# Kernel optimization log

Hardware: AMD Instinct MI355X
Metric: run time of the kernel (lower is better)

## Reference

```python
import jax, jax.numpy as jnp
import numpy as np

# dims: L blocks, S cur_seq, M memory_len, B batch, D embed, H heads, IN input_dim
L, S, M, B, D, H, IN = 4, 512, 512, 8, 1024, 16, 128
HD = D // H
GRU_BIAS = 2.0  # config['gru_bias']


def _ln(x, s, b, eps=1e-5):
    mu = x.mean(-1, keepdims=True)
    var = ((x - mu) ** 2).mean(-1, keepdims=True)
    return (x - mu) * jax.lax.rsqrt(var + eps) * s + b


def _pos_emb(full_seq, dim):
    # SinusoidalPE: freqs = arange(0, dim, 2.0); inv = 10000**(-freqs/dim); seq descending
    freqs = jnp.arange(0, dim, 2.0)
    inv = 10000.0 ** (-freqs / dim)
    seq = jnp.arange(full_seq - 1, -1, -1.0)
    ang = seq[:, None] * inv[None, :]
    return jnp.concatenate([jnp.sin(ang), jnp.cos(ang)], axis=-1)  # (F, dim)


def _rel_shift(x):
    # x: (q, k, b, h) -> Transformer-XL relative shift
    q, k, b, h = x.shape
    xp = jnp.pad(x, ((0, 0), (1, 0), (0, 0), (0, 0)))
    return xp.reshape(k + 1, q, b, h)[1:].reshape(q, k, b, h)


def _gru(x, y, Wr, Ur, Wz, Uz, Wg, Ug):
    r = jax.nn.sigmoid(y @ Wr + x @ Ur)
    z = jax.nn.sigmoid(y @ Wz + x @ Uz - GRU_BIAS)
    hcand = jnp.tanh(y @ Wg + (r * x) @ Ug)
    return (1.0 - z) * x + z * hcand


def setup_inputs() -> dict:
    key = jax.random.key(0)
    ks = iter(jax.random.split(key, 64))

    def mat(*shape):
        return jax.random.normal(next(ks), shape, jnp.float32) * (shape[-2] ** -0.5)

    return dict(
        h=jax.random.normal(next(ks), (B, S, IN), jnp.float32),
        memory=jnp.zeros((L, M, B, D), jnp.float32),
        We=mat(IN, D), be=jnp.zeros((D,), jnp.float32),
        ln1_s=jnp.ones((L, D), jnp.float32), ln1_b=jnp.zeros((L, D), jnp.float32),
        ln2_s=jnp.ones((L, D), jnp.float32), ln2_b=jnp.zeros((L, D), jnp.float32),
        Wq=mat(L, D, D), bq=jnp.zeros((L, D), jnp.float32),
        Wk=mat(L, D, D), bk=jnp.zeros((L, D), jnp.float32),
        Wv=mat(L, D, D), bv=jnp.zeros((L, D), jnp.float32),
        Wr=mat(L, D, D), br=jnp.zeros((L, D), jnp.float32),
        Wo=mat(L, D, D), bo=jnp.zeros((L, D), jnp.float32),
        u=jax.random.normal(next(ks), (L, H, HD), jnp.float32) * 0.02,
        vb=jax.random.normal(next(ks), (L, H, HD), jnp.float32) * 0.02,
        gWr=mat(L, 2, D, D), gUr=mat(L, 2, D, D),
        gWz=mat(L, 2, D, D), gUz=mat(L, 2, D, D),
        gWg=mat(L, 2, D, D), gUg=mat(L, 2, D, D),
        fW1=mat(L, D, 4 * D), fb1=jnp.zeros((L, 4 * D), jnp.float32),
        fW2=mat(L, 4 * D, D), fb2=jnp.zeros((L, D), jnp.float32),
    )


def reference(h, memory, We, be, ln1_s, ln1_b, ln2_s, ln2_b,
              Wq, bq, Wk, bk, Wv, bv, Wr, br, Wo, bo, u, vb,
              gWr, gUr, gWz, gUz, gWg, gUg, fW1, fb1, fW2, fb2):
    x = jnp.transpose(h, (1, 0, 2))                      # (S, B, IN)
    x = jax.nn.gelu(x @ We + be, approximate=False)      # (S, B, D)
    F = S + M
    pos = _pos_emb(F, D)                                 # (F, D)
    mask = jnp.triu(jnp.ones((S, F), bool), k=1 + M)     # (S, F)
    scale = HD ** -0.5
    out = x
    for i in range(L):
        full = jnp.concatenate([memory[i], out], axis=0)  # (F, B, D)
        qn = _ln(out, ln1_s[i], ln1_b[i])
        kn = _ln(full, ln1_s[i], ln1_b[i])
        q = (qn @ Wq[i] + bq[i]).reshape(S, B, H, HD)
        k = (kn @ Wk[i] + bk[i]).reshape(F, B, H, HD)
        v = (kn @ Wv[i] + bv[i]).reshape(F, B, H, HD)
        r = (pos @ Wr[i] + br[i]).reshape(F, H, HD)
        content = jnp.einsum('ibhd,jbhd->ijbh', q + u[i], k)
        position = _rel_shift(jnp.einsum('ibhd,jhd->ijbh', q + vb[i], r))
        attn = (content + position) * scale               # (S, F, B, H)
        attn = jnp.where(mask[:, :, None, None], -1e30, attn)
        a = jax.nn.softmax(attn, axis=1)
        y = jnp.einsum('ijbh,jbhd->ibhd', a, v).reshape(S, B, D) @ Wo[i] + bo[i]
        y = jax.nn.gelu(y, approximate=False)
        out1 = _gru(out, y, gWr[i, 0], gUr[i, 0], gWz[i, 0], gUz[i, 0], gWg[i, 0], gUg[i, 0])
        e = _ln(out1, ln2_s[i], ln2_b[i])
        e = jax.nn.gelu(e @ fW1[i] + fb1[i], approximate=False)
        e = jax.nn.gelu(e @ fW2[i] + fb2[i], approximate=False)
        out = _gru(out1, e, gWr[i, 1], gUr[i, 1], gWz[i, 1], gUz[i, 1], gWg[i, 1], gUg[i, 1])
    return jnp.transpose(out, (1, 0, 2))                  # (B, S, D)
```

## Files before the change

kernel.cpp:

```cpp
#include <hip/hip_runtime.h>

typedef unsigned short u16;
typedef unsigned long long u64;
typedef __attribute__((ext_vector_type(8))) short bf16x8;
typedef __attribute__((ext_vector_type(4))) float f32x4;

#define DEVI __device__ __forceinline__

#define KSC 0.1803368801111244f

DEVI u16 f2b(float f) {
  unsigned u = __float_as_uint(f);
  u += 0x7fffu + ((u >> 16) & 1u);
  return (u16)(u >> 16);
}
DEVI float b2f(u16 v) { return __uint_as_float((unsigned)v << 16); }
DEVI unsigned cvtpk(float lo, float hi) {
  unsigned r;
  asm("v_cvt_pk_bf16_f32 %0, %1, %2" : "=v"(r) : "v"(lo), "v"(hi));
  return r;
}
DEVI float tanh_f(float x) {
  float xc = fminf(fmaxf(x, -15.f), 15.f);
  float e = __expf(2.f * xc);
  return (e - 1.f) / (e + 1.f);
}
DEVI float gelu_f(float x) {
  float u = 0.7978845608028654f * x * (1.f + 0.044715f * x * x);
  return 0.5f * x * (1.f + tanh_f(u));
}
DEVI float sigm_f(float x) { return 1.f / (1.f + __expf(-x)); }

DEVI void gload16(const void* g, void* l) {
  __builtin_amdgcn_global_load_lds((__attribute__((address_space(1))) void*)g,
                                   (__attribute__((address_space(3))) void*)l, 16, 0, 0);
}

template <int NT, int BN>
__global__ __launch_bounds__(NT) void gemm_bt(
    const u16* __restrict__ A, const u16* __restrict__ Bt,
    const float* __restrict__ bias, const float* __restrict__ bias2,
    float* __restrict__ C32, u16* __restrict__ C16, u16* __restrict__ C16b,
    int M, int N, int K, int ldA, int ldB, int ldC,
    long long sA, long long sBb, long long sBh, long long sC, int nH, int flags)
{
  constexpr int WN = BN / 32;
  constexpr int RA = (128 * 8) / NT;
  constexpr int RB = (BN * 8) / NT;
  __shared__ __align__(16) u16 Sm[2][(128 + BN) * 64];
  const int z = blockIdx.z;
  const int zb = z / nH, zh = z - zb * nH;
  A  += (long long)z * sA;
  Bt += (long long)zb * sBb + (long long)zh * sBh;
  const long long cOff = (long long)z * sC;
  const int m0 = blockIdx.x * 128, n0 = blockIdx.y * BN;
  const int t = threadIdx.x, lane = t & 63;
  const int w = t >> 6;
  const int wm = (w / WN) * 64, wn = (w % WN) * 32;

  f32x4 acc[4][2];
#pragma unroll
  for (int i = 0; i < 4; ++i)
#pragma unroll
    for (int j = 0; j < 2; ++j) { f32x4 zz = {0.f, 0.f, 0.f, 0.f}; acc[i][j] = zz; }

  auto stage = [&](int buf, int k0) {
#pragma unroll
    for (int r = 0; r < RA; ++r) {
      const int c = r * NT + t;
      const int row = c >> 3;
      const int col = (c & 7) << 3;
      int ga = m0 + row; if (ga >= M) ga = M - 1;
      gload16(A + (long long)ga * ldA + (k0 + col),
              &Sm[buf][(size_t)(r * NT + (t & (NT - 64))) * 8]);
    }
#pragma unroll
    for (int r = 0; r < RB; ++r) {
      const int c = r * NT + t;
      const int row = c >> 3;
      const int col = (c & 7) << 3;
      int gb = n0 + row; if (gb >= N) gb = N - 1;
      gload16(Bt + (long long)gb * ldB + (k0 + col),
              &Sm[buf][(size_t)(1024 + r * NT + (t & (NT - 64))) * 8]);
    }
  };

  auto compute = [&](int buf) {
    const u16* As = &Sm[buf][0];
    const u16* Bs = &Sm[buf][128 * 64];
#pragma unroll
    for (int ks = 0; ks < 2; ++ks) {
      const int ko = ks * 32 + ((lane >> 4) << 3);
      bf16x8 af[4], bfv[2];
#pragma unroll
      for (int i = 0; i < 4; ++i)
        af[i] = *(const bf16x8*)&As[(wm + i * 16 + (lane & 15)) * 64 + ko];
#pragma unroll
      for (int i = 0; i < 2; ++i)
        bfv[i] = *(const bf16x8*)&Bs[(wn + i * 16 + (lane & 15)) * 64 + ko];
#pragma unroll
      for (int mi = 0; mi < 4; ++mi)
#pragma unroll
        for (int ni = 0; ni < 2; ++ni)
          acc[mi][ni] = __builtin_amdgcn_mfma_f32_16x16x32_bf16(af[mi], bfv[ni], acc[mi][ni], 0, 0, 0);
    }
  };

  stage(0, 0);
  __syncthreads();
  int cur = 0;
  for (int k0 = 64; k0 < K; k0 += 64) {
    stage(cur ^ 1, k0);
    compute(cur);
    __syncthreads();
    cur ^= 1;
  }
  compute(cur);

  const int cb = n0 + wn + (lane & 15);
  const int rb = m0 + wm + ((lane >> 4) << 2);
#pragma unroll
  for (int ni = 0; ni < 2; ++ni) {
    const int col = cb + ni * 16;
    if (col >= N) continue;
    float bv = 0.f;
    if (flags & 2) bv = ((flags & 128) && zh) ? bias2[col] : bias[col];
#pragma unroll
    for (int mi = 0; mi < 4; ++mi) {
#pragma unroll
      for (int q = 0; q < 4; ++q) {
        const int row = rb + mi * 16 + q;
        if (row >= M) continue;
        float x = acc[mi][ni][q] + bv;
        if (flags & 1) x = gelu_f(x);
        if (flags & 64) {
          const long long o = ((long long)((row & 7) * 16 + (col >> 6)) * ldC + (row >> 3)) * 64 + (col & 63);
          C16[o] = f2b(x * KSC);
          C16b[o] = f2b((x + bias2[col]) * KSC);
        } else if (flags & 128) {
          if (zh == 0) {
            const long long o = ((long long)((row & 7) * 16 + (col >> 6)) * ldC + (row >> 3)) * 64 + (col & 63);
            C16[o] = f2b(x);
          } else {
            C16b[(long long)row * 1024 + col] = f2b(x);
          }
        } else {
          long long o;
          if (flags & 16)
            o = ((long long)((row & 7) * 16 + (col >> 6)) * ldC + (row >> 3)) * 64 + (col & 63);
          else if (flags & 32)
            o = ((long long)(col >> 6) * 1024 + row) * 64 + (col & 63);
          else
            o = cOff + (long long)row * ldC + col;
          if (flags & 4) C32[o] = x;
          if (flags & 8) C16[o] = f2b(x);
        }
      }
    }
  }
}

__global__ __launch_bounds__(256) void fused_attn(
    const u16* __restrict__ Qu,
    const u16* __restrict__ Qv,
    const u16* __restrict__ Kb,
    const u16* __restrict__ Vt,
    const u16* __restrict__ Rh,
    u16* __restrict__ Y)
{
  constexpr int F = 1024;
  const int bid = blockIdx.x;
  const int wk = (bid & 7) * 128 + (bid >> 3);
  const int i0 = (wk & 7) * 64;
  const int bh = wk >> 3;
  const int h = bh & 15;

  __shared__ __align__(16) u16 Ks[2][64 * 64];
  __shared__ __align__(16) u16 Vs[2][64 * 64];
  __shared__ __align__(16) u16 Rs[2][64 * 64];
  __shared__ __align__(8) u16 PBT[2][64 * 68];
  __shared__ __align__(16) u16 Ps[4][16][72];

  const int t = threadIdx.x;
  const int lane = t & 63;
  const int wq = t >> 6;
  const int l15 = lane & 15, lhi = lane >> 4;

  const u16* QUg = Qu + ((size_t)bh * 512 + i0) * 64;
  const u16* QVg = Qv + ((size_t)bh * 512 + i0) * 64;
  const u16* Kg = Kb + (size_t)bh * F * 64;
  const u16* Vg = Vt + (size_t)bh * 64 * F;
  const u16* Rg = Rh + (size_t)h * F * 64;

  bf16x8 au[2], av[2];
#pragma unroll
  for (int ks = 0; ks < 2; ++ks) {
    const int arow = wq * 16 + l15;
    au[ks] = *(const bf16x8*)(QUg + arow * 64 + ks * 32 + lhi * 8);
    av[ks] = *(const bf16x8*)(QVg + arow * 64 + ks * 32 + lhi * 8);
  }

  auto stageT = [&](const u16* g, u16* dst) {
#pragma unroll
    for (int rnd = 0; rnd < 2; ++rnd) {
      const int idx = rnd * 256 + t;
      const int row = idx >> 3;
      const int gs = (idx & 7) ^ (row & 7);
      gload16(g + row * 64 + gs * 8, dst + (size_t)(rnd * 256 + (t & 192)) * 8);
    }
  };
  auto stageVf = [&](int j0, u16* dst) {
#pragma unroll
    for (int rnd = 0; rnd < 2; ++rnd) {
      const int idx = rnd * 256 + t;
      const int row = idx >> 3;
      const int gs = (idx & 7) ^ (row & 7);
      gload16(Vg + (size_t)row * F + j0 + gs * 8, dst + (size_t)(rnd * 256 + (t & 192)) * 8);
    }
  };

  const int nT = i0 / 64 + 9;

  stageT(Kg, Ks[0]);
  stageVf(0, Vs[0]);
  stageT(Rg + (size_t)(512 - i0) * 64, Rs[0]);
  stageT(Rg + (size_t)(448 - i0) * 64, Rs[1]);
  __syncthreads();
  {
    f32x4 pb0[4];
#pragma unroll
    for (int i = 0; i < 4; ++i) { f32x4 zz = {0.f, 0.f, 0.f, 0.f}; pb0[i] = zz; }
    __builtin_amdgcn_s_setprio(1);
#pragma unroll
    for (int ks = 0; ks < 2; ++ks)
#pragma unroll
      for (int ni = 0; ni < 4; ++ni) {
        const int brow = ni * 16 + l15;
        const bf16x8 br_ = *(const bf16x8*)&Rs[1][brow * 64 + (((ks * 4 + lhi) ^ (brow & 7)) << 3)];
        pb0[ni] = __builtin_amdgcn_mfma_f32_16x16x32_bf16(av[ks], br_, pb0[ni], 0, 0, 0);
      }
    __builtin_amdgcn_s_setprio(0);
#pragma unroll
    for (int ni = 0; ni < 4; ++ni) {
      u64 w = (u64)cvtpk(pb0[ni][0], pb0[ni][1]) | ((u64)cvtpk(pb0[ni][2], pb0[ni][3]) << 32);
      *(u64*)&PBT[0][(size_t)(ni * 16 + l15) * 68 + wq * 16 + lhi * 4] = w;
    }
  }
  __syncthreads();

  f32x4 Oacc[4];
#pragma unroll
  for (int i = 0; i < 4; ++i) { f32x4 zz = {0.f, 0.f, 0.f, 0.f}; Oacc[i] = zz; }
  float mrow[4] = {-3.0e38f, -3.0e38f, -3.0e38f, -3.0e38f};
  float lrow[4] = {0.f, 0.f, 0.f, 0.f};

  for (int st = 0; st < nT; ++st) {
    const int b = st & 1;
    const bool lastT = (st == nT - 1);

    if (!lastT) {
      const int j1 = (st + 1) * 64;
      stageT(Kg + (size_t)j1 * 64, Ks[b ^ 1]);
      stageVf(j1, Vs[b ^ 1]);
      if (st + 1 < nT - 1)
        stageT(Rg + (size_t)(j1 - i0 + 512) * 64, Rs[b ^ 1]);
    }

    f32x4 cacc[4], pbh[4];
#pragma unroll
    for (int i = 0; i < 4; ++i) {
      f32x4 zz = {0.f, 0.f, 0.f, 0.f};
      cacc[i] = zz; pbh[i] = zz;
    }
    __builtin_amdgcn_s_setprio(1);
#pragma unroll
    for (int ks = 0; ks < 2; ++ks) {
#pragma unroll
      for (int ni = 0; ni < 4; ++ni) {
        const int brow = ni * 16 + l15;
        const bf16x8 bk_ = *(const bf16x8*)&Ks[b][brow * 64 + (((ks * 4 + lhi) ^ (brow & 7)) << 3)];
        cacc[ni] = __builtin_amdgcn_mfma_f32_16x16x32_bf16(au[ks], bk_, cacc[ni], 0, 0, 0);
      }
      if (!lastT) {
#pragma unroll
        for (int ni = 0; ni < 4; ++ni) {
          const int brow = ni * 16 + l15;
          const bf16x8 br_ = *(const bf16x8*)&Rs[b][brow * 64 + (((ks * 4 + lhi) ^ (brow & 7)) << 3)];
          pbh[ni] = __builtin_amdgcn_mfma_f32_16x16x32_bf16(av[ks], br_, pbh[ni], 0, 0, 0);
        }
      }
    }
    __builtin_amdgcn_s_setprio(0);

    if (!lastT) {
#pragma unroll
      for (int ni = 0; ni < 4; ++ni) {
        u64 w = (u64)cvtpk(pbh[ni][0], pbh[ni][1]) | ((u64)cvtpk(pbh[ni][2], pbh[ni][3]) << 32);
        *(u64*)&PBT[(st + 1) & 1][(size_t)(ni * 16 + l15) * 68 + wq * 16 + lhi * 4] = w;
      }
    }

    const u16* pbLo = &PBT[st & 1][0];
    const u16* pbHi = &PBT[(st + 1) & 1][0];
    float sc[4][4];
#pragma unroll
    for (int ni = 0; ni < 4; ++ni) {
      const int dj = ni * 16 + l15;
#pragma unroll
      for (int qq = 0; qq < 4; ++qq) {
        const int di = wq * 16 + lhi * 4 + qq;
        const int cc = dj - di + 63;
        const float pb = b2f((cc < 64) ? pbLo[(size_t)cc * 68 + di]
                                       : pbHi[(size_t)(cc - 64) * 68 + di]);
        float s = cacc[ni][qq] + pb;
        if (lastT && dj > di) s = -1e30f;
        sc[ni][qq] = s;
      }
    }

    float nm[4], esc[4];
#pragma unroll
    for (int qq = 0; qq < 4; ++qq) {
      float r = fmaxf(fmaxf(sc[0][qq], sc[1][qq]), fmaxf(sc[2][qq], sc[3][qq]));
      r = fmaxf(r, __shfl_xor(r, 1));
      r = fmaxf(r, __shfl_xor(r, 2));
      r = fmaxf(r, __shfl_xor(r, 4));
      r = fmaxf(r, __shfl_xor(r, 8));
      nm[qq] = fmaxf(mrow[qq], r);
      esc[qq] = exp2f(mrow[qq] - nm[qq]);
      mrow[qq] = nm[qq];
    }
    float ps[4][4];
    float rsum[4] = {0.f, 0.f, 0.f, 0.f};
#pragma unroll
    for (int ni = 0; ni < 4; ++ni)
#pragma unroll
      for (int qq = 0; qq < 4; ++qq) {
        float p = exp2f(sc[ni][qq] - nm[qq]);
        ps[ni][qq] = p;
        rsum[qq] += p;
      }
#pragma unroll
    for (int qq = 0; qq < 4; ++qq) {
      float r = rsum[qq];
      r += __shfl_xor(r, 1);
      r += __shfl_xor(r, 2);
      r += __shfl_xor(r, 4);
      r += __shfl_xor(r, 8);
      lrow[qq] = lrow[qq] * esc[qq] + r;
    }
#pragma unroll
    for (int nd = 0; nd < 4; ++nd)
#pragma unroll
      for (int qq = 0; qq < 4; ++qq) Oacc[nd][qq] *= esc[qq];

#pragma unroll
    for (int ni = 0; ni < 4; ++ni) {
      unsigned p01 = cvtpk(ps[ni][0], ps[ni][1]);
      unsigned p23 = cvtpk(ps[ni][2], ps[ni][3]);
      Ps[wq][lhi * 4 + 0][ni * 16 + l15] = (u16)p01;
      Ps[wq][lhi * 4 + 1][ni * 16 + l15] = (u16)(p01 >> 16);
      Ps[wq][lhi * 4 + 2][ni * 16 + l15] = (u16)p23;
      Ps[wq][lhi * 4 + 3][ni * 16 + l15] = (u16)(p23 >> 16);
    }
    __builtin_amdgcn_s_setprio(1);
#pragma unroll
    for (int ks = 0; ks < 2; ++ks) {
      const bf16x8 pa = *(const bf16x8*)&Ps[wq][l15][ks * 32 + lhi * 8];
#pragma unroll
      for (int nd = 0; nd < 4; ++nd) {
        const int vrow = nd * 16 + l15;
        const bf16x8 vb_ = *(const bf16x8*)&Vs[b][vrow * 64 + (((ks * 4 + lhi) ^ (vrow & 7)) << 3)];
        Oacc[nd] = __builtin_amdgcn_mfma_f32_16x16x32_bf16(pa, vb_, Oacc[nd], 0, 0, 0);
      }
    }
    __builtin_amdgcn_s_setprio(0);

    __syncthreads();
  }

  float inv[4];
#pragma unroll
  for (int qq = 0; qq < 4; ++qq) inv[qq] = 1.f / lrow[qq];
  const int b = bh >> 4;
  const int rbase = i0 + wq * 16 + lhi * 4;
#pragma unroll
  for (int nd = 0; nd < 4; ++nd) {
    const int d = nd * 16 + l15;
    unsigned w01 = cvtpk(Oacc[nd][0] * inv[0], Oacc[nd][1] * inv[1]);
    unsigned w23 = cvtpk(Oacc[nd][2] * inv[2], Oacc[nd][3] * inv[3]);
    u16* yb = Y + (size_t)rbase * 8192 + b * 1024 + h * 64 + d;
    yb[0] = (u16)w01; yb[8192] = (u16)(w01 >> 16);
    yb[16384] = (u16)w23; yb[24576] = (u16)(w23 >> 16);
  }
}

__global__ __launch_bounds__(256) void biasprep(const float* __restrict__ bq,
                                                const float* __restrict__ u,
                                                const float* __restrict__ vb,
                                                float* __restrict__ bqu,
                                                float* __restrict__ dvb)
{
  const int i = blockIdx.x * 256 + threadIdx.x;
  bqu[i] = bq[i] + u[i];
  dvb[i] = vb[i] - u[i];
}

#define MAXW 20
struct WPack {
  const float* src[MAXW];
  u16* dst[MAXW];
  int K[MAXW], N[MAXW];
  int tilePrefix[MAXW + 1];
  int nm;
};

__global__ __launch_bounds__(256) void wtrans_kernel(WPack p) {
  int bid = blockIdx.x;
  int m = 0;
  while (m < p.nm && bid >= p.tilePrefix[m + 1]) ++m;
  if (m >= p.nm) return;
  const int lt = bid - p.tilePrefix[m];
  const int K = p.K[m], N = p.N[m];
  const int tN = N >> 5;
  const int kt = lt / tN, nt = lt - kt * tN;
  const int k0 = kt << 5, n0 = nt << 5;
  const float* src = p.src[m];
  u16* dst = p.dst[m];
  __shared__ float tile[32][33];
  const int t = threadIdx.x;
  const int r = t >> 3, c4 = (t & 7) << 2;
  float4 v = *(const float4*)&src[(size_t)(k0 + r) * N + n0 + c4];
  tile[r][c4 + 0] = v.x; tile[r][c4 + 1] = v.y; tile[r][c4 + 2] = v.z; tile[r][c4 + 3] = v.w;
  __syncthreads();
  u16 o0 = f2b(tile[c4 + 0][r]);
  u16 o1 = f2b(tile[c4 + 1][r]);
  u16 o2 = f2b(tile[c4 + 2][r]);
  u16 o3 = f2b(tile[c4 + 3][r]);
  u64 w = (u64)o0 | ((u64)o1 << 16) | ((u64)o2 << 32) | ((u64)o3 << 48);
  *(u64*)&dst[(size_t)(n0 + r) * K + k0 + c4] = w;
}

__global__ __launch_bounds__(256) void ln_kernel(
    const float* __restrict__ Xmem, const float* __restrict__ Xout, int rowsMem,
    const float* __restrict__ sc, const float* __restrict__ bi, u16* __restrict__ dst)
{
  const int row = blockIdx.x;
  const float* src = (row < rowsMem) ? (Xmem + (long long)row * 1024)
                                     : (Xout + (long long)(row - rowsMem) * 1024);
  const int t = threadIdx.x;
  float4 v = *(const float4*)&src[t * 4];
  float s1 = v.x + v.y + v.z + v.w;
  float s2 = v.x * v.x + v.y * v.y + v.z * v.z + v.w * v.w;
#pragma unroll
  for (int o = 32; o > 0; o >>= 1) { s1 += __shfl_down(s1, o); s2 += __shfl_down(s2, o); }
  __shared__ float red[8];
  const int wv = t >> 6;
  if ((t & 63) == 0) { red[wv * 2] = s1; red[wv * 2 + 1] = s2; }
  __syncthreads();
  s1 = red[0] + red[2] + red[4] + red[6];
  s2 = red[1] + red[3] + red[5] + red[7];
  const float mu = s1 * (1.f / 1024.f);
  const float var = s2 * (1.f / 1024.f) - mu * mu;
  const float rs = rsqrtf(var + 1e-5f);
  float vals[4] = {v.x, v.y, v.z, v.w};
  u16 o4[4];
#pragma unroll
  for (int j = 0; j < 4; ++j) {
    const int c = t * 4 + j;
    o4[j] = f2b((vals[j] - mu) * rs * sc[c] + bi[c]);
  }
  *(u64*)&dst[(long long)row * 1024 + t * 4] =
      (u64)o4[0] | ((u64)o4[1] << 16) | ((u64)o4[2] << 32) | ((u64)o4[3] << 48);
}

__global__ __launch_bounds__(256) void prep_vt16(const u16* __restrict__ Vf, u16* __restrict__ VT)
{
  const int f0 = blockIdx.x * 64;
  const int bh = blockIdx.y;
  const int b = bh >> 4, h = bh & 15;
  __shared__ u16 tl[64 * 64];
  const int t = threadIdx.x;
  {
    const int fr = t >> 2, c0 = (t & 3) * 16;
    const u16* src = Vf + ((size_t)(f0 + fr) * 8 + b) * 1024 + h * 64 + c0;
    *(bf16x8*)&tl[fr * 64 + c0] = *(const bf16x8*)src;
    *(bf16x8*)&tl[fr * 64 + c0 + 8] = *(const bf16x8*)(src + 8);
  }
  __syncthreads();
  {
    const int dr = t >> 2, c0 = (t & 3) * 16;
    u16* dst = VT + ((long long)bh * 64 + dr) * 1024 + f0 + c0;
#pragma unroll
    for (int j = 0; j < 16; ++j) dst[j] = tl[(c0 + j) * 64 + dr];
  }
}

__global__ __launch_bounds__(256) void pe_kernel(u16* __restrict__ PEB)
{
  const long long idx = (long long)blockIdx.x * 256 + threadIdx.x;
  const int p = (int)(idx >> 10);
  const int d = idx & 1023;
  const int q = d & 511;
  const float inv = powf(10000.f, -(float)(2 * q) * (1.f / 1024.f));
  const float ang = (float)(1023 - p) * inv;
  PEB[idx] = f2b((d < 512) ? sinf(ang) : cosf(ang));
}

__global__ __launch_bounds__(256) void embed_conv(const float* __restrict__ h, u16* __restrict__ A)
{
  const long long idx = (long long)blockIdx.x * 256 + threadIdx.x;
  const int c = idx & 127;
  const int r = (int)(idx >> 7);
  const int s = r >> 3, b = r & 7;
  A[idx] = f2b(h[(((long long)b * 512 + s) << 7) + c]);
}

__global__ __launch_bounds__(256) void gru_elemA(const u16* __restrict__ T1, u16* __restrict__ T2,
                                                 const float* __restrict__ X, u16* __restrict__ RXBF)
{
  const long long i8 = ((long long)blockIdx.x * 256 + threadIdx.x) * 8;
  const int row = (int)(i8 >> 10);
  const int c = i8 & 1023;
  const u16* t1 = T1 + (long long)row * 3072 + c;
  u16* t2 = T2 + (long long)row * 2048 + c;
  bf16x8 ry = *(const bf16x8*)t1;
  bf16x8 zy = *(const bf16x8*)(t1 + 1024);
  bf16x8 rx = *(const bf16x8*)t2;
  bf16x8 zx = *(const bf16x8*)(t2 + 1024);
  float4 x0 = *(const float4*)(X + i8);
  float4 x1 = *(const float4*)(X + i8 + 4);
  float xs[8] = {x0.x, x0.y, x0.z, x0.w, x1.x, x1.y, x1.z, x1.w};
  u16 ro[8], zo[8];
#pragma unroll
  for (int j = 0; j < 8; ++j) {
    float r = sigm_f(b2f((u16)ry[j]) + b2f((u16)rx[j]));
    float z = sigm_f(b2f((u16)zy[j]) + b2f((u16)zx[j]) - 2.f);
    ro[j] = f2b(r * xs[j]);
    zo[j] = f2b(z);
  }
  *(u64*)&RXBF[i8] = (u64)ro[0] | ((u64)ro[1] << 16) | ((u64)ro[2] << 32) | ((u64)ro[3] << 48);
  *(u64*)&RXBF[i8 + 4] = (u64)ro[4] | ((u64)ro[5] << 16) | ((u64)ro[6] << 32) | ((u64)ro[7] << 48);
  *(u64*)&t2[0] = (u64)zo[0] | ((u64)zo[1] << 16) | ((u64)zo[2] << 32) | ((u64)zo[3] << 48);
  *(u64*)&t2[4] = (u64)zo[4] | ((u64)zo[5] << 16) | ((u64)zo[6] << 32) | ((u64)zo[7] << 48);
}

__global__ __launch_bounds__(256) void gru_elemB(const u16* __restrict__ T1, const u16* __restrict__ T2,
                                                 const u16* __restrict__ TG, const float* __restrict__ X,
                                                 float* __restrict__ O, u16* __restrict__ XBF)
{
  const long long i8 = ((long long)blockIdx.x * 256 + threadIdx.x) * 8;
  const int row = (int)(i8 >> 10);
  const int c = i8 & 1023;
  bf16x8 gy = *(const bf16x8*)(T1 + (long long)row * 3072 + 2048 + c);
  bf16x8 tt = *(const bf16x8*)(TG + i8);
  bf16x8 zz = *(const bf16x8*)(T2 + (long long)row * 2048 + c);
  float4 x0 = *(const float4*)(X + i8);
  float4 x1 = *(const float4*)(X + i8 + 4);
  float xs[8] = {x0.x, x0.y, x0.z, x0.w, x1.x, x1.y, x1.z, x1.w};
  float os[8];
  u16 ob[8];
#pragma unroll
  for (int j = 0; j < 8; ++j) {
    float z = b2f((u16)zz[j]);
    float o = (1.f - z) * xs[j] + z * tanh_f(b2f((u16)gy[j]) + b2f((u16)tt[j]));
    os[j] = o;
    ob[j] = f2b(o);
  }
  float4 o0 = {os[0], os[1], os[2], os[3]};
  float4 o1 = {os[4], os[5], os[6], os[7]};
  *(float4*)(O + i8) = o0;
  *(float4*)(O + i8 + 4) = o1;
  *(u64*)&XBF[i8] = (u64)ob[0] | ((u64)ob[1] << 16) | ((u64)ob[2] << 32) | ((u64)ob[3] << 48);
  *(u64*)&XBF[i8 + 4] = (u64)ob[4] | ((u64)ob[5] << 16) | ((u64)ob[6] << 32) | ((u64)ob[7] << 48);
}

__global__ __launch_bounds__(256) void out_transpose(const float* __restrict__ O, float* __restrict__ dst)
{
  const long long i4 = ((long long)blockIdx.x * 256 + threadIdx.x) * 4;
  const int d = i4 & 1023;
  const int r = (int)(i4 >> 10);
  const int s = r >> 3, b = r & 7;
  float4 v = *(const float4*)(O + i4);
  *(float4*)&dst[(((long long)b * 512 + s) << 10) + d] = v;
}

extern "C" void kernel_launch(void* const* d_in, const int* in_sizes, int n_in,
                              void* d_out, int out_size, void* d_ws, size_t ws_size,
                              hipStream_t stream)
{
  (void)in_sizes; (void)n_in; (void)out_size; (void)ws_size;
  const float* h_in   = (const float*)d_in[0];
  const float* memory = (const float*)d_in[1];
  const float* We     = (const float*)d_in[2];
  const float* be     = (const float*)d_in[3];
  const float* ln1s   = (const float*)d_in[4];
  const float* ln1b   = (const float*)d_in[5];
  const float* ln2s   = (const float*)d_in[6];
  const float* ln2b   = (const float*)d_in[7];
  const float* Wq     = (const float*)d_in[8];
  const float* bq     = (const float*)d_in[9];
  const float* Wk     = (const float*)d_in[10];
  const float* bk     = (const float*)d_in[11];
  const float* Wv     = (const float*)d_in[12];
  const float* bv     = (const float*)d_in[13];
  const float* Wr     = (const float*)d_in[14];
  const float* br     = (const float*)d_in[15];
  const float* Wo     = (const float*)d_in[16];
  const float* bo     = (const float*)d_in[17];
  const float* uu     = (const float*)d_in[18];
  const float* vbp    = (const float*)d_in[19];
  const float* gWr    = (const float*)d_in[20];
  const float* gUr    = (const float*)d_in[21];
  const float* gWz    = (const float*)d_in[22];
  const float* gUz    = (const float*)d_in[23];
  const float* gWg    = (const float*)d_in[24];
  const float* gUg    = (const float*)d_in[25];
  const float* fW1    = (const float*)d_in[26];
  const float* fb1    = (const float*)d_in[27];
  const float* fW2    = (const float*)d_in[28];
  const float* fb2    = (const float*)d_in[29];

  constexpr int S = 512, MM = 512, B = 8, D = 1024, H = 16, IN = 128, F = 1024;
  constexpr int SB = 4096, FB = 8192;
  constexpr long long DD = (long long)D * D;

  char* ws = (char*)d_ws;
  size_t off = 0;
  auto alloc = [&](size_t bytes) -> size_t {
    size_t o = off; off = (off + bytes + 255) & ~(size_t)255; return o;
  };
  const size_t oWT   = alloc((size_t)25 * DD * 2);
  const size_t oWET  = alloc((size_t)D * IN * 2);
  const size_t oPEB  = alloc((size_t)F * D * 2);
  const size_t oOUT  = alloc((size_t)SB * D * 4);
  const size_t oOUT1 = alloc((size_t)SB * D * 4);
  const size_t oXBF  = alloc((size_t)SB * D * 2);
  const size_t oYBF  = alloc((size_t)SB * D * 2);
  const size_t oYBFA = alloc((size_t)SB * D * 2);
  const size_t oABUF = alloc((size_t)SB * D * 2);
  const size_t oKN   = alloc((size_t)FB * D * 2);
  const size_t oQU   = alloc((size_t)B * H * S * 64 * 2);
  const size_t oQV   = alloc((size_t)B * H * S * 64 * 2);
  const size_t oKBH  = alloc((size_t)B * H * F * 64 * 2);
  const size_t oVT   = alloc((size_t)B * H * F * 64 * 2);
  const size_t oRH   = alloc((size_t)H * F * 64 * 2);
  const size_t oBQU  = alloc((size_t)D * 4);
  const size_t oDVB  = alloc((size_t)D * 4);
  const size_t oUNI  = off;

  u16* WTp   = (u16*)(ws + oWT);
  u16* WETp  = (u16*)(ws + oWET);
  u16* PEBp  = (u16*)(ws + oPEB);
  float* OUTp  = (float*)(ws + oOUT);
  float* OUT1p = (float*)(ws + oOUT1);
  u16* XBFp  = (u16*)(ws + oXBF);
  u16* YBFp  = (u16*)(ws + oYBF);
  u16* YBFAp = (u16*)(ws + oYBFA);
  u16* ABUFp = (u16*)(ws + oABUF);
  u16* KNp   = (u16*)(ws + oKN);
  u16* QUp   = (u16*)(ws + oQU);
  u16* QVp   = (u16*)(ws + oQV);
  u16* KBHp  = (u16*)(ws + oKBH);
  u16* VTp   = (u16*)(ws + oVT);
  u16* RHp   = (u16*)(ws + oRH);
  float* bquP = (float*)(ws + oBQU);
  float* dvbP = (float*)(ws + oDVB);
  u16* VF16p  = (u16*)(ws + oUNI);
  u16* T1p    = (u16*)(ws + oUNI);
  u16* T2p    = (u16*)(ws + oUNI + (size_t)SB * 3 * D * 2 + 256);
  u16* TGp    = (u16*)(ws + oUNI + (size_t)SB * 5 * D * 2 + 512);
  u16* FFNBp  = (u16*)(ws + oUNI);

  auto gemm = [&](const u16* A, const u16* Bt, const float* bias, const float* bias2,
                  float* C32, u16* C16, u16* C16b,
                  int M, int N, int K, int ldA, int ldB, int ldC,
                  long long sA, long long sBb, long long sBh, long long sC, int nH, int Z,
                  int flags) {
    if (M >= 2048 && N >= 1024 && (N % 128) == 0) {
      dim3 grid((M + 127) / 128, N / 128, Z);
      gemm_bt<512, 128><<<grid, 512, 0, stream>>>(A, Bt, bias, bias2, C32, C16, C16b,
                                                  M, N, K, ldA, ldB, ldC,
                                                  sA, sBb, sBh, sC, nH, flags);
    } else {
      dim3 grid((M + 127) / 128, (N + 63) / 64, Z);
      gemm_bt<256, 64><<<grid, 256, 0, stream>>>(A, Bt, bias, bias2, C32, C16, C16b,
                                                 M, N, K, ldA, ldB, ldC,
                                                 sA, sBb, sBh, sC, nH, flags);
    }
  };

  pe_kernel<<<(F * D) / 256, 256, 0, stream>>>(PEBp);
  {
    WPack p{};
    p.nm = 1; p.src[0] = We; p.dst[0] = WETp; p.K[0] = IN; p.N[0] = D;
    p.tilePrefix[0] = 0; p.tilePrefix[1] = (IN / 32) * (D / 32);
    wtrans_kernel<<<p.tilePrefix[1], 256, 0, stream>>>(p);
  }
  embed_conv<<<(SB * IN) / 256, 256, 0, stream>>>(h_in, ABUFp);
  gemm(ABUFp, WETp, be, nullptr, OUTp, XBFp, nullptr, SB, D, IN, IN, IN, D,
       0, 0, 0, 0, 1, 1, 1 | 2 | 4 | 8);

  for (int li = 0; li < 4; ++li) {
    WPack p{};
    int nt = 0, id = 0;
    auto addw = [&](const float* s, u16* d, int K, int N) {
      p.src[id] = s; p.dst[id] = d; p.K[id] = K; p.N[id] = N;
      p.tilePrefix[id] = nt; nt += (K / 32) * (N / 32); ++id;
    };
    addw(Wq + li * DD, WTp + 0 * DD, D, D);
    addw(Wk + li * DD, WTp + 1 * DD, D, D);
    addw(Wv + li * DD, WTp + 2 * DD, D, D);
    addw(Wr + li * DD, WTp + 3 * DD, D, D);
    addw(Wo + li * DD, WTp + 4 * DD, D, D);
    addw(gWr + (li * 2 + 0) * DD, WTp + 5 * DD, D, D);
    addw(gWz + (li * 2 + 0) * DD, WTp + 6 * DD, D, D);
    addw(gWg + (li * 2 + 0) * DD, WTp + 7 * DD, D, D);
    addw(gUr + (li * 2 + 0) * DD, WTp + 8 * DD, D, D);
    addw(gUz + (li * 2 + 0) * DD, WTp + 9 * DD, D, D);
    addw(gUg + (li * 2 + 0) * DD, WTp + 10 * DD, D, D);
    addw(gWr + (li * 2 + 1) * DD, WTp + 11 * DD, D, D);
    addw(gWz + (li * 2 + 1) * DD, WTp + 12 * DD, D, D);
    addw(gWg + (li * 2 + 1) * DD, WTp + 13 * DD, D, D);
    addw(gUr + (li * 2 + 1) * DD, WTp + 14 * DD, D, D);
    addw(gUz + (li * 2 + 1) * DD, WTp + 15 * DD, D, D);
    addw(gUg + (li * 2 + 1) * DD, WTp + 16 * DD, D, D);
    addw(fW1 + li * (long long)D * 4096, WTp + 17 * DD, D, 4096);
    addw(fW2 + li * (long long)4096 * D, WTp + 21 * DD, 4096, D);
    p.tilePrefix[id] = nt; p.nm = id;
    wtrans_kernel<<<nt, 256, 0, stream>>>(p);

    ln_kernel<<<FB, 256, 0, stream>>>(memory + (long long)li * MM * B * D, OUTp, MM * B,
                                      ln1s + li * D, ln1b + li * D, KNp);
    const u16* QN = KNp + (size_t)MM * B * D;

    biasprep<<<4, 256, 0, stream>>>(bq + li * D, uu + li * D, vbp + li * D, bquP, dvbP);
    gemm(QN, WTp + 0 * DD, bquP, dvbP, nullptr, QUp, QVp, SB, D, D, D, D,  S,
         0, 0, 0, 0, 1, 1, 2 | 64);
    gemm(KNp, WTp + 1 * DD, bk + li * D, bv + li * D, nullptr, KBHp, VF16p,
         FB, D, D, D, D,  F, 0, 0, DD, 0, 2, 2, 2 | 128);
    prep_vt16<<<dim3(F / 64, B * H), 256, 0, stream>>>(VF16p, VTp);
    gemm(PEBp, WTp + 3 * DD, br + li * D, nullptr, nullptr, RHp, nullptr,
         F, D, D, D, D, D, 0, 0, 0, 0, 1, 1, 2 | 8 | 32);

    fused_attn<<<dim3((S / 64) * B * H), 256, 0, stream>>>(QUp, QVp, KBHp, VTp, RHp, YBFAp);

    gemm(YBFAp, WTp + 4 * DD, bo + li * D, nullptr, nullptr, YBFp, nullptr,
         SB, D, D, D, D, D, 0, 0, 0, 0, 1, 1, 1 | 2 | 8);

    gemm(YBFp, WTp + 5 * DD, nullptr, nullptr, nullptr, T1p, nullptr,
         SB, 3 * D, D, D, D, 3 * D, 0, 0, 0, 0, 1, 1, 8);
    gemm(XBFp, WTp + 8 * DD, nullptr, nullptr, nullptr, T2p, nullptr,
         SB, 2 * D, D, D, D, 2 * D, 0, 0, 0, 0, 1, 1, 8);
    gru_elemA<<<(SB * D / 8) / 256, 256, 0, stream>>>(T1p, T2p, OUTp, ABUFp);
    gemm(ABUFp, WTp + 10 * DD, nullptr, nullptr, nullptr, TGp, nullptr,
         SB, D, D, D, D, D, 0, 0, 0, 0, 1, 1, 8);
    gru_elemB<<<(SB * D / 8) / 256, 256, 0, stream>>>(T1p, T2p, TGp, OUTp, OUT1p, XBFp);

    ln_kernel<<<SB, 256, 0, stream>>>(OUT1p, OUT1p, SB, ln2s + li * D, ln2b + li * D, ABUFp);
    gemm(ABUFp, WTp + 17 * DD, fb1 + li * 4096, nullptr, nullptr, FFNBp, nullptr,
         SB, 4096, D, D, D, 4096, 0, 0, 0, 0, 1, 1, 1 | 2 | 8);
    gemm(FFNBp, WTp + 21 * DD, fb2 + li * D, nullptr, nullptr, YBFp, nullptr,
         SB, D, 4096, 4096, 4096, D, 0, 0, 0, 0, 1, 1, 1 | 2 | 8);

    gemm(YBFp, WTp + 11 * DD, nullptr, nullptr, nullptr, T1p, nullptr,
         SB, 3 * D, D, D, D, 3 * D, 0, 0, 0, 0, 1, 1, 8);
    gemm(XBFp, WTp + 14 * DD, nullptr, nullptr, nullptr, T2p, nullptr,
         SB, 2 * D, D, D, D, 2 * D, 0, 0, 0, 0, 1, 1, 8);
    gru_elemA<<<(SB * D / 8) / 256, 256, 0, stream>>>(T1p, T2p, OUT1p, ABUFp);
    gemm(ABUFp, WTp + 16 * DD, nullptr, nullptr, nullptr, TGp, nullptr,
         SB, D, D, D, D, D, 0, 0, 0, 0, 1, 1, 8);
    gru_elemB<<<(SB * D / 8) / 256, 256, 0, stream>>>(T1p, T2p, TGp, OUT1p, OUTp, XBFp);
  }

  out_transpose<<<(SB * D / 4) / 256, 256, 0, stream>>>(OUTp, (float*)d_out);
}
```

Before: 2.887 ms.

## Fuse GRU gate elementwise ops and output transpose into GEMM epilogues

The GRU r/z gate computation moves into the epilogue of the U-projection GEMM, and the candidate/blend step into the epilogue of the Ug GEMM. This removes the gru_elemA/gru_elemB kernels and the intermediate T2/TG buffers. On the last layer the output permutation to (B,S,D) is written directly from the epilogue, so out_transpose is dropped. In exchange, the epilogues now do scalar non-vectorized gathers from E1/EX, which could cost more per element than the vectorized standalone kernels.

Measured after the change: 3.091 ms. 1.07x slower.

```diff
diff --git a/kernel.cpp b/kernel.cpp
--- a/kernel.cpp
+++ b/kernel.cpp
@@ -40,6 +40,8 @@
 __global__ __launch_bounds__(NT) void gemm_bt(
     const u16* __restrict__ A, const u16* __restrict__ Bt,
     const float* __restrict__ bias, const float* __restrict__ bias2,
+    const u16* __restrict__ E1, const u16* __restrict__ E2,
+    const float* __restrict__ EX,
     float* __restrict__ C32, u16* __restrict__ C16, u16* __restrict__ C16b,
     int M, int N, int K, int ldA, int ldB, int ldC,
     long long sA, long long sBb, long long sBh, long long sC, int nH, int flags)
@@ -133,7 +135,28 @@
         if (row >= M) continue;
         float x = acc[mi][ni][q] + bv;
         if (flags & 1) x = gelu_f(x);
-        if (flags & 64) {
+        if (flags & 256) {
+          const float t1v = b2f(E1[(size_t)row * 3072 + col]);
+          if (col < 1024) {
+            const float r = sigm_f(x + t1v);
+            C16[(size_t)row * 1024 + col] = f2b(r * EX[(size_t)row * 1024 + col]);
+          } else {
+            const float zv = sigm_f(x + t1v - 2.f);
+            C16b[(size_t)row * 1024 + col - 1024] = f2b(zv);
+          }
+        } else if (flags & 512) {
+          const float gy = b2f(E1[(size_t)row * 3072 + 2048 + col]);
+          const float zv = b2f(E2[(size_t)row * 1024 + col]);
+          const float xv = EX[(size_t)row * 1024 + col];
+          const float o = (1.f - zv) * xv + zv * tanh_f(x + gy);
+          long long oo;
+          if (flags & 1024)
+            oo = ((((long long)(row & 7) * 512 + (row >> 3))) << 10) + col;
+          else
+            oo = (long long)row * 1024 + col;
+          C32[oo] = o;
+          C16[(size_t)row * 1024 + col] = f2b(o);
+        } else if (flags & 64) {
           const long long o = ((long long)((row & 7) * 16 + (col >> 6)) * ldC + (row >> 3)) * 64 + (col & 63);
           C16[o] = f2b(x * KSC);
           C16b[o] = f2b((x + bias2[col]) * KSC);
@@ -514,75 +537,6 @@
   const int r = (int)(idx >> 7);
   const int s = r >> 3, b = r & 7;
   A[idx] = f2b(h[(((long long)b * 512 + s) << 7) + c]);
-}
-
-__global__ __launch_bounds__(256) void gru_elemA(const u16* __restrict__ T1, u16* __restrict__ T2,
-                                                 const float* __restrict__ X, u16* __restrict__ RXBF)
-{
-  const long long i8 = ((long long)blockIdx.x * 256 + threadIdx.x) * 8;
-  const int row = (int)(i8 >> 10);
-  const int c = i8 & 1023;
-  const u16* t1 = T1 + (long long)row * 3072 + c;
-  u16* t2 = T2 + (long long)row * 2048 + c;
-  bf16x8 ry = *(const bf16x8*)t1;
-  bf16x8 zy = *(const bf16x8*)(t1 + 1024);
-  bf16x8 rx = *(const bf16x8*)t2;
-  bf16x8 zx = *(const bf16x8*)(t2 + 1024);
-  float4 x0 = *(const float4*)(X + i8);
-  float4 x1 = *(const float4*)(X + i8 + 4);
-  float xs[8] = {x0.x, x0.y, x0.z, x0.w, x1.x, x1.y, x1.z, x1.w};
-  u16 ro[8], zo[8];
-#pragma unroll
-  for (int j = 0; j < 8; ++j) {
-    float r = sigm_f(b2f((u16)ry[j]) + b2f((u16)rx[j]));
-    float z = sigm_f(b2f((u16)zy[j]) + b2f((u16)zx[j]) - 2.f);
-    ro[j] = f2b(r * xs[j]);
-    zo[j] = f2b(z);
-  }
-  *(u64*)&RXBF[i8] = (u64)ro[0] | ((u64)ro[1] << 16) | ((u64)ro[2] << 32) | ((u64)ro[3] << 48);
-  *(u64*)&RXBF[i8 + 4] = (u64)ro[4] | ((u64)ro[5] << 16) | ((u64)ro[6] << 32) | ((u64)ro[7] << 48);
-  *(u64*)&t2[0] = (u64)zo[0] | ((u64)zo[1] << 16) | ((u64)zo[2] << 32) | ((u64)zo[3] << 48);
-  *(u64*)&t2[4] = (u64)zo[4] | ((u64)zo[5] << 16) | ((u64)zo[6] << 32) | ((u64)zo[7] << 48);
-}
-
-__global__ __launch_bounds__(256) void gru_elemB(const u16* __restrict__ T1, const u16* __restrict__ T2,
-                                                 const u16* __restrict__ TG, const float* __restrict__ X,
-                                                 float* __restrict__ O, u16* __restrict__ XBF)
-{
-  const long long i8 = ((long long)blockIdx.x * 256 + threadIdx.x) * 8;
-  const int row = (int)(i8 >> 10);
-  const int c = i8 & 1023;
-  bf16x8 gy = *(const bf16x8*)(T1 + (long long)row * 3072 + 2048 + c);
-  bf16x8 tt = *(const bf16x8*)(TG + i8);
-  bf16x8 zz = *(const bf16x8*)(T2 + (long long)row * 2048 + c);
-  float4 x0 = *(const float4*)(X + i8);
-  float4 x1 = *(const float4*)(X + i8 + 4);
-  float xs[8] = {x0.x, x0.y, x0.z, x0.w, x1.x, x1.y, x1.z, x1.w};
-  float os[8];
-  u16 ob[8];
-#pragma unroll
-  for (int j = 0; j < 8; ++j) {
-    float z = b2f((u16)zz[j]);
-    float o = (1.f - z) * xs[j] + z * tanh_f(b2f((u16)gy[j]) + b2f((u16)tt[j]));
-    os[j] = o;
-    ob[j] = f2b(o);
-  }
-  float4 o0 = {os[0], os[1], os[2], os[3]};
-  float4 o1 = {os[4], os[5], os[6], os[7]};
-  *(float4*)(O + i8) = o0;
-  *(float4*)(O + i8 + 4) = o1;
-  *(u64*)&XBF[i8] = (u64)ob[0] | ((u64)ob[1] << 16) | ((u64)ob[2] << 32) | ((u64)ob[3] << 48);
-  *(u64*)&XBF[i8 + 4] = (u64)ob[4] | ((u64)ob[5] << 16) | ((u64)ob[6] << 32) | ((u64)ob[7] << 48);
-}
-
-__global__ __launch_bounds__(256) void out_transpose(const float* __restrict__ O, float* __restrict__ dst)
-{
-  const long long i4 = ((long long)blockIdx.x * 256 + threadIdx.x) * 4;
-  const int d = i4 & 1023;
-  const int r = (int)(i4 >> 10);
-  const int s = r >> 3, b = r & 7;
-  float4 v = *(const float4*)(O + i4);
-  *(float4*)&dst[(((long long)b * 512 + s) << 10) + d] = v;
 }
 
 extern "C" void kernel_launch(void* const* d_in, const int* in_sizes, int n_in,
@@ -639,6 +593,7 @@
   const size_t oYBF  = alloc((size_t)SB * D * 2);
   const size_t oYBFA = alloc((size_t)SB * D * 2);
   const size_t oABUF = alloc((size_t)SB * D * 2);
+  const size_t oT2Z  = alloc((size_t)SB * D * 2);
   const size_t oKN   = alloc((size_t)FB * D * 2);
   const size_t oQU   = alloc((size_t)B * H * S * 64 * 2);
   const size_t oQV   = alloc((size_t)B * H * S * 64 * 2);
@@ -658,6 +613,7 @@
   u16* YBFp  = (u16*)(ws + oYBF);
   u16* YBFAp = (u16*)(ws + oYBFA);
   u16* ABUFp = (u16*)(ws + oABUF);
+  u16* T2Zp  = (u16*)(ws + oT2Z);
   u16* KNp   = (u16*)(ws + oKN);
   u16* QUp   = (u16*)(ws + oQU);
   u16* QVp   = (u16*)(ws + oQV);
@@ -668,24 +624,23 @@
   float* dvbP = (float*)(ws + oDVB);
   u16* VF16p  = (u16*)(ws + oUNI);
   u16* T1p    = (u16*)(ws + oUNI);
-  u16* T2p    = (u16*)(ws + oUNI + (size_t)SB * 3 * D * 2 + 256);
-  u16* TGp    = (u16*)(ws + oUNI + (size_t)SB * 5 * D * 2 + 512);
-  u16* FFNBp  = (u16*)(ws + oUNI);
+  u16* FFNBp  = (u16*)(ws + oUNI + (size_t)SB * 3 * D * 2 + 256);
 
   auto gemm = [&](const u16* A, const u16* Bt, const float* bias, const float* bias2,
+                  const u16* E1, const u16* E2, const float* EX,
                   float* C32, u16* C16, u16* C16b,
                   int M, int N, int K, int ldA, int ldB, int ldC,
                   long long sA, long long sBb, long long sBh, long long sC, int nH, int Z,
                   int flags) {
     if (M >= 2048 && N >= 1024 && (N % 128) == 0) {
       dim3 grid((M + 127) / 128, N / 128, Z);
-      gemm_bt<512, 128><<<grid, 512, 0, stream>>>(A, Bt, bias, bias2, C32, C16, C16b,
-                                                  M, N, K, ldA, ldB, ldC,
+      gemm_bt<512, 128><<<grid, 512, 0, stream>>>(A, Bt, bias, bias2, E1, E2, EX,
+                                                  C32, C16, C16b, M, N, K, ldA, ldB, ldC,
                                                   sA, sBb, sBh, sC, nH, flags);
     } else {
       dim3 grid((M + 127) / 128, (N + 63) / 64, Z);
-      gemm_bt<256, 64><<<grid, 256, 0, stream>>>(A, Bt, bias, bias2, C32, C16, C16b,
-                                                 M, N, K, ldA, ldB, ldC,
+      gemm_bt<256, 64><<<grid, 256, 0, stream>>>(A, Bt, bias, bias2, E1, E2, EX,
+                                                 C32, C16, C16b, M, N, K, ldA, ldB, ldC,
                                                  sA, sBb, sBh, sC, nH, flags);
     }
   };
@@ -698,8 +653,8 @@
     wtrans_kernel<<<p.tilePrefix[1], 256, 0, stream>>>(p);
   }
   embed_conv<<<(SB * IN) / 256, 256, 0, stream>>>(h_in, ABUFp);
-  gemm(ABUFp, WETp, be, nullptr, OUTp, XBFp, nullptr, SB, D, IN, IN, IN, D,
-       0, 0, 0, 0, 1, 1, 1 | 2 | 4 | 8);
+  gemm(ABUFp, WETp, be, nullptr, nullptr, nullptr, nullptr, OUTp, XBFp, nullptr,
+       SB, D, IN, IN, IN, D, 0, 0, 0, 0, 1, 1, 1 | 2 | 4 | 8);
 
   for (int li = 0; li < 4; ++li) {
     WPack p{};
@@ -735,43 +690,38 @@
     const u16* QN = KNp + (size_t)MM * B * D;
 
     biasprep<<<4, 256, 0, stream>>>(bq + li * D, uu + li * D, vbp + li * D, bquP, dvbP);
-    gemm(QN, WTp + 0 * DD, bquP, dvbP, nullptr, QUp, QVp, SB, D, D, D, D,  S,
-         0, 0, 0, 0, 1, 1, 2 | 64);
-    gemm(KNp, WTp + 1 * DD, bk + li * D, bv + li * D, nullptr, KBHp, VF16p,
-         FB, D, D, D, D,  F, 0, 0, DD, 0, 2, 2, 2 | 128);
+    gemm(QN, WTp + 0 * DD, bquP, dvbP, nullptr, nullptr, nullptr, nullptr, QUp, QVp,
+         SB, D, D, D, D,  S, 0, 0, 0, 0, 1, 1, 2 | 64);
+    gemm(KNp, WTp + 1 * DD, bk + li * D, bv + li * D, nullptr, nullptr, nullptr,
+         nullptr, KBHp, VF16p, FB, D, D, D, D,  F, 0, 0, DD, 0, 2, 2, 2 | 128);
     prep_vt16<<<dim3(F / 64, B * H), 256, 0, stream>>>(VF16p, VTp);
-    gemm(PEBp, WTp + 3 * DD, br + li * D, nullptr, nullptr, RHp, nullptr,
-         F, D, D, D, D, D, 0, 0, 0, 0, 1, 1, 2 | 8 | 32);
+    gemm(PEBp, WTp + 3 * DD, br + li * D, nullptr, nullptr, nullptr, nullptr,
+         nullptr, RHp, nullptr, F, D, D, D, D, D, 0, 0, 0, 0, 1, 1, 2 | 8 | 32);
 
     fused_attn<<<dim3((S / 64) * B * H), 256, 0, stream>>>(QUp, QVp, KBHp, VTp, RHp, YBFAp);
 
-    gemm(YBFAp, WTp + 4 * DD, bo + li * D, nullptr, nullptr, YBFp, nullptr,
-         SB, D, D, D, D, D, 0, 0, 0, 0, 1, 1, 1 | 2 | 8);
-
-    gemm(YBFp, WTp + 5 * DD, nullptr, nullptr, nullptr, T1p, nullptr,
-         SB, 3 * D, D, D, D, 3 * D, 0, 0, 0, 0, 1, 1, 8);
-    gemm(XBFp, WTp + 8 * DD, nullptr, nullptr, nullptr, T2p, nullptr,
-         SB, 2 * D, D, D, D, 2 * D, 0, 0, 0, 0, 1, 1, 8);
-    gru_elemA<<<(SB * D / 8) / 256, 256, 0, stream>>>(T1p, T2p, OUTp, ABUFp);
-    gemm(ABUFp, WTp + 10 * DD, nullptr, nullptr, nullptr, TGp, nullptr,
-         SB, D, D, D, D, D, 0, 0, 0, 0, 1, 1, 8);
-    gru_elemB<<<(SB * D / 8) / 256, 256, 0, stream>>>(T1p, T2p, TGp, OUTp, OUT1p, XBFp);
+    gemm(YBFAp, WTp + 4 * DD, bo + li * D, nullptr, nullptr, nullptr, nullptr,
+         nullptr, YBFp, nullptr, SB, D, D, D, D, D, 0, 0, 0, 0, 1, 1, 1 | 2 | 8);
+
+    gemm(YBFp, WTp + 5 * DD, nullptr, nullptr, nullptr, nullptr, nullptr,
+         nullptr, T1p, nullptr, SB, 3 * D, D, D, D, 3 * D, 0, 0, 0, 0, 1, 1, 8);
+    gemm(XBFp, WTp + 8 * DD, nullptr, nullptr, T1p, nullptr, OUTp,
+         nullptr, ABUFp, T2Zp, SB, 2 * D, D, D, D, 2 * D, 0, 0, 0, 0, 1, 1, 256);
+    gemm(ABUFp, WTp + 10 * DD, nullptr, nullptr, T1p, T2Zp, OUTp,
+         OUT1p, XBFp, nullptr, SB, D, D, D, D, D, 0, 0, 0, 0, 1, 1, 512);
 
     ln_kernel<<<SB, 256, 0, stream>>>(OUT1p, OUT1p, SB, ln2s + li * D, ln2b + li * D, ABUFp);
-    gemm(ABUFp, WTp + 17 * DD, fb1 + li * 4096, nullptr, nullptr, FFNBp, nullptr,
-         SB, 4096, D, D, D, 4096, 0, 0, 0, 0, 1, 1, 1 | 2 | 8);
-    gemm(FFNBp, WTp + 21 * DD, fb2 + li * D, nullptr, nullptr, YBFp, nullptr,
-         SB, D, 4096, 4096, 4096, D, 0, 0, 0, 0, 1, 1, 1 | 2 | 8);
-
-    gemm(YBFp, WTp + 11 * DD, nullptr, nullptr, nullptr, T1p, nullptr,
-         SB, 3 * D, D, D, D, 3 * D, 0, 0, 0, 0, 1, 1, 8);
-    gemm(XBFp, WTp + 14 * DD, nullptr, nullptr, nullptr, T2p, nullptr,
-         SB, 2 * D, D, D, D, 2 * D, 0, 0, 0, 0, 1, 1, 8);
-    gru_elemA<<<(SB * D / 8) / 256, 256, 0, stream>>>(T1p, T2p, OUT1p, ABUFp);
-    gemm(ABUFp, WTp + 16 * DD, nullptr, nullptr, nullptr, TGp, nullptr,
-         SB, D, D, D, D, D, 0, 0, 0, 0, 1, 1, 8);
-    gru_elemB<<<(SB * D / 8) / 256, 256, 0, stream>>>(T1p, T2p, TGp, OUT1p, OUTp, XBFp);
-  }
-
-  out_transpose<<<(SB * D / 4) / 256, 256, 0, stream>>>(OUTp, (float*)d_out);
-}
+    gemm(ABUFp, WTp + 17 * DD, fb1 + li * 4096, nullptr, nullptr, nullptr, nullptr,
+         nullptr, FFNBp, nullptr, SB, 4096, D, D, D, 4096, 0, 0, 0, 0, 1, 1, 1 | 2 | 8);
+    gemm(FFNBp, WTp + 21 * DD, fb2 + li * D, nullptr, nullptr, nullptr, nullptr,
+         nullptr, YBFp, nullptr, SB, D, 4096, 4096, 4096, D, 0, 0, 0, 0, 1, 1, 1 | 2 | 8);
+
+    gemm(YBFp, WTp + 11 * DD, nullptr, nullptr, nullptr, nullptr, nullptr,
+         nullptr, T1p, nullptr, SB, 3 * D, D, D, D, 3 * D, 0, 0, 0, 0, 1, 1, 8);
+    gemm(XBFp, WTp + 14 * DD, nullptr, nullptr, T1p, nullptr, OUT1p,
+         nullptr, ABUFp, T2Zp, SB, 2 * D, D, D, D, 2 * D, 0, 0, 0, 0, 1, 1, 256);
+    gemm(ABUFp, WTp + 16 * DD, nullptr, nullptr, T1p, T2Zp, OUT1p,
+         (li == 3) ? (float*)d_out : OUTp, XBFp, nullptr,
+         SB, D, D, D, D, D, 0, 0, 0, 0, 1, 1, (li == 3) ? (512 | 1024) : 512);
+  }
+}
```
